# Performance work log

Measured on AMD Instinct MI355X. Metric: run time of the kernel, lower is better.

The kernel has to match this reference:

```python
import jax, jax.numpy as jnp
import numpy as np

N = 8192        # nodes
V = 50000       # vocab = len(dict_node_names)
EMB = 256       # embedding_dim
XI = EMB // 2   # x_increased_dim = 128
DIN = EMB + XI  # 384, SelfAtt_ dim
H = 4           # n_heads
D = 128         # WGAT output_dim per head (fusion dim)
E = 131072      # edges
CHUNK = 32768   # chunk_size (E % CHUNK == 0)


def _ln(x, g, b, eps=1e-5):
    m = jnp.mean(x, axis=-1, keepdims=True)
    v = jnp.mean((x - m) ** 2, axis=-1, keepdims=True)
    return (x - m) * jax.lax.rsqrt(v + eps) * g + b


def _wgat(emb, src, dst, edge_attr, wi, bi, wj, bj, wt, bt, attn):
    # x_i = features at destination (aggregation target), x_j = source/neighbor
    x_i = emb[dst]                                   # [E, din]
    x_j = emb[src]                                   # [E, din]
    h = (x_i @ wi + bi).reshape(E, H, D) + (x_j @ wj + bj).reshape(E, H, D)
    a = jnp.einsum('ehd,hd->eh', h, attn)            # [E, H]
    a = a * edge_attr[:, None]                       # edge weights pre-softmax
    # faithful chunked softmax: normalize over edges WITHIN each chunk (dim=0 per chunk)
    a = jax.nn.softmax(a.reshape(E // CHUNK, CHUNK, H), axis=1).reshape(E, H)
    xt = (x_j @ wt + bt).reshape(E, H, D)            # [E, H, D]
    msg = jnp.einsum('ehd,eh->ed', xt, a)            # sum over heads -> [E, D]
    return jax.ops.segment_sum(msg, dst, num_segments=N)  # aggr='add'


def _emb_forward(ids, edge_index, x, edge_attr, embed,
                 qkv_w, qkv_b, proj_w, proj_b, fuse_w, fuse_b, ln1_g, ln1_b,
                 wi0, bi0, wj0, bj0, wt0, bt0, attn0, skip0_w, skip0_b,
                 wi1, bi1, wj1, bj1, wt1, bt1, attn1, skip1_w, skip1_b,
                 ln2_g, ln2_b):
    E_i = embed[ids]                                 # [N, EMB] gather
    z = jnp.concatenate([jnp.tile(x, (1, XI)), E_i], axis=-1)   # [N, DIN]
    # SelfAtt_ : full N x N attention over nodes, scale = DIN**-0.5
    qkv = z @ qkv_w + qkv_b
    q, k, v = jnp.split(qkv, 3, axis=-1)
    att = jax.nn.softmax((q @ k.T) * (DIN ** -0.5), axis=-1) @ v
    z = att @ proj_w + proj_b                        # [N, DIN]
    emb = jax.nn.silu(_ln(z @ fuse_w + fuse_b, ln1_g, ln1_b)) + E_i  # [N, EMB]
    src, dst = edge_index[0], edge_index[1]
    emb = _wgat(emb, src, dst, edge_attr, wi0, bi0, wj0, bj0, wt0, bt0, attn0)  # [N, D]
    s0 = emb @ skip0_w + skip0_b
    emb = _wgat(emb, src, dst, edge_attr, wi1, bi1, wj1, bj1, wt1, bt1, attn1)  # [N, D]
    s1 = emb @ skip1_w + skip1_b
    emb = _ln(emb + (s0 + s1) * 0.5, ln2_g, ln2_b)
    return emb


def setup_inputs() -> dict:
    key = jax.random.key(0)
    ks = jax.random.split(key, 32)

    def w(k, shape, scale=0.05):
        return jax.random.normal(k, shape, jnp.float32) * scale

    inp = {}
    inp['ids'] = jax.random.randint(ks[0], (N,), 0, V)
    inp['x'] = jax.random.normal(ks[1], (N, 1), jnp.float32)
    inp['edge_attr'] = jax.random.uniform(ks[2], (E,), jnp.float32)
    inp['edge_index'] = jax.random.randint(ks[3], (2, E), 0, N)
    inp['embed'] = w(ks[4], (V, EMB), 1.0)
    inp['qkv_w'] = w(ks[5], (DIN, 3 * DIN)); inp['qkv_b'] = jnp.zeros((3 * DIN,), jnp.float32)
    inp['proj_w'] = w(ks[6], (DIN, DIN));    inp['proj_b'] = jnp.zeros((DIN,), jnp.float32)
    inp['fuse_w'] = w(ks[7], (DIN, EMB));    inp['fuse_b'] = jnp.zeros((EMB,), jnp.float32)
    inp['ln1_g'] = jnp.ones((EMB,), jnp.float32); inp['ln1_b'] = jnp.zeros((EMB,), jnp.float32)
    # WGAT layer 0: in=EMB, out=D per head, H heads
    inp['wi0'] = w(ks[8], (EMB, H * D));  inp['bi0'] = jnp.zeros((H * D,), jnp.float32)
    inp['wj0'] = w(ks[9], (EMB, H * D));  inp['bj0'] = jnp.zeros((H * D,), jnp.float32)
    inp['wt0'] = w(ks[10], (EMB, H * D)); inp['bt0'] = jnp.zeros((H * D,), jnp.float32)
    inp['attn0'] = w(ks[11], (H, D), 0.1)
    inp['skip0_w'] = w(ks[12], (D, D));   inp['skip0_b'] = jnp.zeros((D,), jnp.float32)
    # WGAT layer 1: in=D
    inp['wi1'] = w(ks[13], (D, H * D));   inp['bi1'] = jnp.zeros((H * D,), jnp.float32)
    inp['wj1'] = w(ks[14], (D, H * D));   inp['bj1'] = jnp.zeros((H * D,), jnp.float32)
    inp['wt1'] = w(ks[15], (D, H * D));   inp['bt1'] = jnp.zeros((H * D,), jnp.float32)
    inp['attn1'] = w(ks[16], (H, D), 0.1)
    inp['skip1_w'] = w(ks[17], (D, D));   inp['skip1_b'] = jnp.zeros((D,), jnp.float32)
    inp['ln2_g'] = jnp.ones((D,), jnp.float32); inp['ln2_b'] = jnp.zeros((D,), jnp.float32)
    return inp


def reference(ids, x, edge_attr, edge_index, embed,
              qkv_w, qkv_b, proj_w, proj_b, fuse_w, fuse_b, ln1_g, ln1_b,
              wi0, bi0, wj0, bj0, wt0, bt0, attn0, skip0_w, skip0_b,
              wi1, bi1, wj1, bj1, wt1, bt1, attn1, skip1_w, skip1_b,
              ln2_g, ln2_b):
    emb = _emb_forward(ids, edge_index, x, edge_attr, embed,
                       qkv_w, qkv_b, proj_w, proj_b, fuse_w, fuse_b, ln1_g, ln1_b,
                       wi0, bi0, wj0, bj0, wt0, bt0, attn0, skip0_w, skip0_b,
                       wi1, bi1, wj1, bj1, wt1, bt1, attn1, skip1_w, skip1_b,
                       ln2_g, ln2_b)
    return (emb, embed, ids)
```

## Files before the change

kernel.cpp:

```cpp
#include <hip/hip_runtime.h>

typedef __attribute__((ext_vector_type(8))) short bfrag;
typedef __attribute__((ext_vector_type(4))) float f4;

#define MFMA(a,b,c) __builtin_amdgcn_mfma_f32_16x16x32_bf16(a,b,c,0,0,0)

__device__ __forceinline__ unsigned short f2b(float x){
  union { float f; unsigned int u; } v; v.f = x;
  unsigned int r = v.u + 0x7fffu + ((v.u >> 16) & 1u);
  return (unsigned short)(r >> 16);
}
__device__ __forceinline__ float b2f(unsigned short h){
  union { unsigned int u; float f; } v; v.u = ((unsigned int)h) << 16;
  return v.f;
}

__global__ __launch_bounds__(256) void k_prep(
    const float* __restrict__ qkv_w, const float* __restrict__ proj_w,
    const float* __restrict__ proj_b, const float* __restrict__ fuse_w,
    const float* __restrict__ fuse_b,
    const float* __restrict__ wt0,
    const float* __restrict__ wt1, const float* __restrict__ sk0w,
    const float* __restrict__ wi0, const float* __restrict__ bi0,
    const float* __restrict__ wj0, const float* __restrict__ bj0,
    const float* __restrict__ wi1, const float* __restrict__ bi1,
    const float* __restrict__ wj1, const float* __restrict__ bj1,
    const float* __restrict__ attn0, const float* __restrict__ attn1,
    const float* __restrict__ bt0, const float* __restrict__ bt1,
    const float* __restrict__ sk0b,
    const float* __restrict__ embed, const int* __restrict__ ids,
    unsigned short* __restrict__ BtQKV, unsigned short* __restrict__ BtW2,
    unsigned short* __restrict__ BtT0, unsigned short* __restrict__ BtT1,
    float* __restrict__ biasW2,
    float* __restrict__ biasT0, float* __restrict__ biasT1,
    float* __restrict__ wsum, float* __restrict__ Ei)
{
  int b = blockIdx.x, t = threadIdx.x;
  if (b < 1152) {
    int idx = b*256 + t; int k = idx/1152, n = idx - k*1152;
    BtQKV[(size_t)n*256 + k] = f2b(qkv_w[128*1152 + idx]);
  } else if (b < 1536) {
    int k = b - 1152;
    float s = 0.f;
    for (int j = 0; j < 384; ++j) s += proj_w[(size_t)k*384 + j] * fuse_w[(size_t)j*256 + t];
    BtW2[(size_t)t*384 + k] = f2b(s);
  } else if (b == 1536) {
    float s = fuse_b[t];
    for (int j = 0; j < 384; ++j) s += proj_b[j] * fuse_w[(size_t)j*256 + t];
    biasW2[t] = s;
  } else if (b < 2049) {
    int idx = (b-1537)*256 + t; int k = idx/512, n = idx - k*512;
    BtT0[(size_t)n*256 + k] = f2b(wt0[idx]);
  } else if (b < 2305) {
    int idx = (b-2049)*256 + t; int k = idx/512, n = idx - k*512;
    BtT1[(size_t)n*128 + k] = f2b(wt1[idx]);
  } else if (b < 2369) {
    int idx = (b-2305)*256 + t; int k = idx/128, n = idx - k*128;
    BtT1[(size_t)(512+n)*128 + k] = f2b(sk0w[idx]);
  } else if (b < 2373) {
    int idx = (b-2369)*256 + t;
    int h = idx >> 8, k = idx & 255;
    float s = 0.f;
    for (int d = 0; d < 128; ++d) s += wi0[(size_t)k*512 + h*128 + d] * attn0[h*128 + d];
    BtT0[(size_t)(512 + h)*256 + k] = f2b(s);
    if (idx < 4) {
      float sb = 0.f;
      for (int d = 0; d < 128; ++d) sb += bi0[idx*128 + d] * attn0[idx*128 + d];
      biasT0[512 + idx] = sb;
    }
  } else if (b < 2377) {
    int idx = (b-2373)*256 + t;
    int h = idx >> 8, k = idx & 255;
    float s = 0.f;
    for (int d = 0; d < 128; ++d) s += wj0[(size_t)k*512 + h*128 + d] * attn0[h*128 + d];
    BtT0[(size_t)(516 + h)*256 + k] = f2b(s);
    if (idx < 4) {
      float sb = 0.f;
      for (int d = 0; d < 128; ++d) sb += bj0[idx*128 + d] * attn0[idx*128 + d];
      biasT0[516 + idx] = sb;
    }
  } else if (b < 2379) {
    int idx = (b-2377)*256 + t;
    int h = idx >> 7, k = idx & 127;
    float s = 0.f;
    for (int d = 0; d < 128; ++d) s += wi1[(size_t)k*512 + h*128 + d] * attn1[h*128 + d];
    BtT1[(size_t)(640 + h)*128 + k] = f2b(s);
    if (idx < 4) {
      float sb = 0.f;
      for (int d = 0; d < 128; ++d) sb += bi1[idx*128 + d] * attn1[idx*128 + d];
      biasT1[640 + idx] = sb;
    }
  } else if (b < 2381) {
    int idx = (b-2379)*256 + t;
    int h = idx >> 7, k = idx & 127;
    float s = 0.f;
    for (int d = 0; d < 128; ++d) s += wj1[(size_t)k*512 + h*128 + d] * attn1[h*128 + d];
    BtT1[(size_t)(644 + h)*128 + k] = f2b(s);
    if (idx < 4) {
      float sb = 0.f;
      for (int d = 0; d < 128; ++d) sb += bj1[idx*128 + d] * attn1[idx*128 + d];
      biasT1[644 + idx] = sb;
    }
  } else if (b < 2383) {
    int idx = (b-2381)*256 + t; biasT0[idx] = bt0[idx];
  } else if (b < 2385) {
    int idx = (b-2383)*256 + t; biasT1[idx] = bt1[idx];
  } else if (b == 2385) {
    if (t < 128) biasT1[512 + t] = sk0b[t];
  } else if (b < 2391) {
    int n = (b-2386)*256 + t;
    if (n < 1152) {
      float s = 0.f;
      for (int k = 0; k < 128; ++k) s += qkv_w[(size_t)k*1152 + n];
      wsum[n] = s;
    }
  } else {
    int idx = (b-2391)*256 + t;
    int n = idx >> 6, c4 = idx & 63;
    reinterpret_cast<float4*>(Ei)[idx] =
        reinterpret_cast<const float4*>(embed + (size_t)ids[n]*256)[c4];
  }
}

__global__ void k_outcopy(const float* __restrict__ embed, const int* __restrict__ ids,
                          float* __restrict__ out){
  int i = blockIdx.x*256 + threadIdx.x;
  if (i < 3200000)
    reinterpret_cast<float4*>(out)[262144 + i] = reinterpret_cast<const float4*>(embed)[i];
  if (i < 8192) out[13848576 + i] = (float)ids[i];
}

__global__ void k_deg(const int* __restrict__ ei, int* __restrict__ deg){
  int e = blockIdx.x*256 + threadIdx.x; if (e >= 131072) return;
  atomicAdd(&deg[ei[131072 + e]], 1);
}

__global__ __launch_bounds__(1024) void k_scan(const int* __restrict__ deg,
                                               int* __restrict__ off, int* __restrict__ cursor){
  int t = threadIdx.x;
  int v[8]; int s = 0;
  #pragma unroll
  for (int i=0;i<8;++i){ v[i] = s; s += deg[t*8 + i]; }
  int lane = t & 63, w = t >> 6;
  int si = s;
  for (int o=1;o<64;o<<=1){ int u = __shfl_up(si, o); if (lane >= o) si += u; }
  __shared__ int wsum[16];
  if (lane == 63) wsum[w] = si;
  __syncthreads();
  if (t < 16) {
    int x = wsum[t];
    for (int o=1;o<16;o<<=1){ int u = __shfl_up(x, o); if (t >= o) x += u; }
    wsum[t] = x;
  }
  __syncthreads();
  int wbase = (w == 0) ? 0 : wsum[w-1];
  int base = wbase + (si - s);
  #pragma unroll
  for (int i=0;i<8;++i){ int o2 = base + v[i]; off[t*8+i] = o2; cursor[t*8+i] = o2; }
  if (t == 1023) off[8192] = wbase + si;
}

__global__ void k_fill(const int* __restrict__ ei, int* __restrict__ cursor,
                       int* __restrict__ elist){
  int e = blockIdx.x*256 + threadIdx.x; if (e >= 131072) return;
  int d = ei[131072 + e];
  int slot = atomicAdd(&cursor[d], 1);
  elist[slot] = e;
}

__global__ __launch_bounds__(256) void k_gemm(
    const float* __restrict__ A, int lda,
    const unsigned short* __restrict__ Bt, int K,
    const float* __restrict__ bias,
    float* __restrict__ C, int ldc, int mode,
    const float* __restrict__ xv, const float* __restrict__ wsum,
    unsigned short* __restrict__ qO, unsigned short* __restrict__ kO,
    unsigned short* __restrict__ vO,
    const unsigned short* __restrict__ opA, const float* __restrict__ cw)
{
  __shared__ unsigned short As[128*40];
  __shared__ unsigned short Bs[128*40];
  const int t = threadIdx.x;
  const int wid = t >> 6, l = t & 63;
  const int lr = l & 15, lg = l >> 4;
  const int arow0 = blockIdx.y*128, bn0 = blockIdx.x*128;
  const int wr = (wid >> 1)*64, wc = (wid & 1)*64;
  f4 zero = {0.f,0.f,0.f,0.f};
  f4 acc[4][4];
  #pragma unroll
  for (int i=0;i<4;++i)
    #pragma unroll
    for (int j=0;j<4;++j) acc[i][j] = zero;

  for (int k0 = 0; k0 < K; k0 += 32) {
    #pragma unroll
    for (int p=0;p<4;++p) {
      int row = p*32 + (t>>3);
      int c4  = (t&7)*4;
      ushort4 h4;
      if (mode == 2) {
        const float* w4 = &cw[(arow0+row)*4];
        float a0=0.f,a1=0.f,a2=0.f,a3=0.f;
        #pragma unroll
        for (int s=0;s<4;++s) {
          ushort4 u = *reinterpret_cast<const ushort4*>(
              opA + (size_t)s*3145728 + (size_t)(arow0+row)*384 + k0 + c4);
          float wv = w4[s];
          a0 += b2f(u.x)*wv; a1 += b2f(u.y)*wv; a2 += b2f(u.z)*wv; a3 += b2f(u.w)*wv;
        }
        h4.x = f2b(a0); h4.y = f2b(a1); h4.z = f2b(a2); h4.w = f2b(a3);
      } else {
        float4 v = *reinterpret_cast<const float4*>(A + (size_t)(arow0+row)*lda + k0 + c4);
        h4.x = f2b(v.x); h4.y = f2b(v.y); h4.z = f2b(v.z); h4.w = f2b(v.w);
      }
      *reinterpret_cast<ushort4*>(&As[row*40 + c4]) = h4;
    }
    #pragma unroll
    for (int p=0;p<2;++p) {
      int n  = p*64 + (t>>2);
      int c8 = (t&3)*8;
      int4 v = *reinterpret_cast<const int4*>(Bt + (size_t)(bn0+n)*K + k0 + c8);
      *reinterpret_cast<int4*>(&Bs[n*40 + c8]) = v;
    }
    __syncthreads();
    bfrag af[4], bfm[4];
    #pragma unroll
    for (int mi=0;mi<4;++mi) af[mi] = *reinterpret_cast<const bfrag*>(&As[(wr+mi*16+lr)*40 + lg*8]);
    #pragma unroll
    for (int ni=0;ni<4;++ni) bfm[ni] = *reinterpret_cast<const bfrag*>(&Bs[(wc+ni*16+lr)*40 + lg*8]);
    #pragma unroll
    for (int mi=0;mi<4;++mi)
      #pragma unroll
      for (int ni=0;ni<4;++ni)
        acc[mi][ni] = MFMA(af[mi], bfm[ni], acc[mi][ni]);
    __syncthreads();
  }
  #pragma unroll
  for (int mi=0;mi<4;++mi) {
    #pragma unroll
    for (int ni=0;ni<4;++ni) {
      int col = bn0 + wc + ni*16 + lr;
      float bv = bias[col];
      float wsv = (mode==1) ? wsum[col] : 0.f;
      #pragma unroll
      for (int i=0;i<4;++i) {
        int row = arow0 + wr + mi*16 + lg*4 + i;
        float val = acc[mi][ni][i] + bv;
        if (mode == 1) {
          val += xv[row]*wsv;
          if (col < 384) val *= 0.05103103631f;
          unsigned short hv = f2b(val);
          if (col < 384)      qO[(size_t)row*384 + col] = hv;
          else if (col < 768) kO[(size_t)row*384 + col - 384] = hv;
          else {
            int d = col - 768, j = row;
            size_t vidx = (size_t)(j >> 5)*12288 + (size_t)(d >> 4)*512
                        + (size_t)(d & 15)*32 + (size_t)((j & 31) >> 3)*8 + (j & 7);
            vO[vidx] = hv;
          }
        } else {
          C[(size_t)row*ldc + col] = val;
        }
      }
    }
  }
}

__global__ __launch_bounds__(256,2) void k_flash(
    const unsigned short* __restrict__ qg,
    const unsigned short* __restrict__ kg,
    const unsigned short* __restrict__ vg,
    unsigned short* __restrict__ Opart, float* __restrict__ mpart, float* __restrict__ lpart)
{
  __shared__ unsigned short Ks[32*384];
  __shared__ unsigned short Ps[64*40];
  __shared__ float f_s[64];

  const int t = threadIdx.x;
  const int w = t >> 6, l = t & 63;
  const int lr = l & 15, lg = l >> 4;
  const int qbi = blockIdx.x >> 2, split = blockIdx.x & 3;
  const int qbase = qbi * 64;

  #define STAGE_K(JJ) do { \
    _Pragma("unroll") \
    for (int p_=0;p_<6;++p_) { \
      int idx_ = p_*256 + t; \
      int row_ = idx_ / 48, uu_ = idx_ - row_*48; \
      int ug_ = uu_ ^ (row_ & 7); \
      const unsigned short* gp_ = kg + (size_t)((JJ) + row_)*384 + ug_*8; \
      __builtin_amdgcn_global_load_lds((const __attribute__((address_space(1))) void*)gp_, \
          (__attribute__((address_space(3))) void*)&Ks[idx_*8], 16, 0, 0); \
    } } while(0)

  bfrag qf[12];
  #pragma unroll
  for (int kk=0;kk<12;++kk)
    qf[kk] = *reinterpret_cast<const bfrag*>(qg + (size_t)(qbase + w*16 + lr)*384 + kk*32 + lg*8);

  f4 zero = {0.f,0.f,0.f,0.f};
  f4 o[4][6];
  #pragma unroll
  for (int a=0;a<4;++a)
    #pragma unroll
    for (int b=0;b<6;++b) o[a][b] = zero;

  float m = -3e38f, lsum = 0.f;
  const int j0beg = split*2048, jend = j0beg + 2048;

  STAGE_K(j0beg);
  __syncthreads();

  for (int j0 = j0beg; j0 < jend; j0 += 32) {
    f4 s0 = zero, s1 = zero;
    __builtin_amdgcn_s_setprio(1);
    #pragma unroll
    for (int kk=0;kk<12;++kk) {
      int su = ((kk*4 + lg) ^ (lr & 7)) * 8;
      bfrag k0 = *reinterpret_cast<const bfrag*>(&Ks[lr*384 + su]);
      bfrag k1 = *reinterpret_cast<const bfrag*>(&Ks[(16+lr)*384 + su]);
      s0 = MFMA(k0, qf[kk], s0);
      s1 = MFMA(k1, qf[kk], s1);
    }
    __builtin_amdgcn_s_setprio(0);

    float mt = fmaxf(fmaxf(fmaxf(s0[0],s0[1]),fmaxf(s0[2],s0[3])),
                     fmaxf(fmaxf(s1[0],s1[1]),fmaxf(s1[2],s1[3])));
    mt = fmaxf(mt, __shfl_xor(mt,16));
    mt = fmaxf(mt, __shfl_xor(mt,32));
    bool grew = mt > m + 8.f;
    bool doresc = __any(grew);
    float mn = doresc ? fmaxf(m, mt) : m;
    float p0[4], p1[4];
    float sum = 0.f;
    #pragma unroll
    for (int i=0;i<4;++i) {
      p0[i] = __expf(s0[i]-mn); p1[i] = __expf(s1[i]-mn);
      sum += p0[i] + p1[i];
    }
    sum += __shfl_xor(sum,16);
    sum += __shfl_xor(sum,32);
    float f = 1.f;
    if (doresc) {
      f = __expf(m - mn);
      lsum = lsum * f + sum;
      m = mn;
    } else {
      lsum += sum;
    }

    unsigned int pk0 = (unsigned int)f2b(p0[0]) | ((unsigned int)f2b(p0[1]) << 16);
    unsigned int pk1 = (unsigned int)f2b(p0[2]) | ((unsigned int)f2b(p0[3]) << 16);
    unsigned int pk2 = (unsigned int)f2b(p1[0]) | ((unsigned int)f2b(p1[1]) << 16);
    unsigned int pk3 = (unsigned int)f2b(p1[2]) | ((unsigned int)f2b(p1[3]) << 16);
    int prow = (w*16 + lr)*40;
    *reinterpret_cast<unsigned int*>(&Ps[prow + lg*4])          = pk0;
    *reinterpret_cast<unsigned int*>(&Ps[prow + lg*4 + 2])      = pk1;
    *reinterpret_cast<unsigned int*>(&Ps[prow + 16 + lg*4])     = pk2;
    *reinterpret_cast<unsigned int*>(&Ps[prow + 16 + lg*4 + 2]) = pk3;
    if (lg == 0) f_s[w*16 + lr] = f;

    __syncthreads();

    if (j0 + 32 < jend) STAGE_K(j0 + 32);

    const int jt = j0 >> 5;
    bfrag vf[6];
    #pragma unroll
    for (int dt=0;dt<6;++dt)
      vf[dt] = *reinterpret_cast<const bfrag*>(
          vg + (size_t)jt*12288 + (size_t)(w*6 + dt)*512 + lr*32 + lg*8);

    bfrag pf[4];
    #pragma unroll
    for (int qt=0;qt<4;++qt)
      pf[qt] = *reinterpret_cast<const bfrag*>(&Ps[(qt*16+lr)*40 + lg*8]);
    #pragma unroll
    for (int qt=0;qt<4;++qt) {
      #pragma unroll
      for (int i=0;i<4;++i) {
        float frv = f_s[qt*16 + lg*4 + i];
        #pragma unroll
        for (int dt=0;dt<6;++dt) o[qt][dt][i] *= frv;
      }
    }
    __builtin_amdgcn_s_setprio(1);
    #pragma unroll
    for (int qt=0;qt<4;++qt)
      #pragma unroll
      for (int dt=0;dt<6;++dt)
        o[qt][dt] = MFMA(pf[qt], vf[dt], o[qt][dt]);
    __builtin_amdgcn_s_setprio(0);

    __syncthreads();
  }
  #undef STAGE_K

  unsigned short* Op = Opart + (size_t)split*8192*384;
  #pragma unroll
  for (int qt=0;qt<4;++qt)
    #pragma unroll
    for (int dt=0;dt<6;++dt)
      #pragma unroll
      for (int i=0;i<4;++i)
        Op[(size_t)(qbase + qt*16 + lg*4 + i)*384 + w*96 + dt*16 + lr] = f2b(o[qt][dt][i]);
  if (lg == 0) {
    mpart[split*8192 + qbase + w*16 + lr] = m;
    lpart[split*8192 + qbase + w*16 + lr] = lsum;
  }
}

__global__ void k_cw(const float* __restrict__ mp, const float* __restrict__ lp,
                     float* __restrict__ cw)
{
  int r = blockIdx.x*256 + threadIdx.x;
  float m0 = mp[r], m1 = mp[8192+r], m2 = mp[16384+r], m3 = mp[24576+r];
  float M = fmaxf(fmaxf(m0,m1), fmaxf(m2,m3));
  float w0 = __expf(m0-M), w1 = __expf(m1-M), w2 = __expf(m2-M), w3 = __expf(m3-M);
  float L = lp[r]*w0 + lp[8192+r]*w1 + lp[16384+r]*w2 + lp[24576+r]*w3;
  float inv = 1.f / L;
  float4 o4 = make_float4(w0*inv, w1*inv, w2*inv, w3*inv);
  *reinterpret_cast<float4*>(&cw[r*4]) = o4;
}

__global__ __launch_bounds__(256) void k_ln1(const float* __restrict__ pre, const float* __restrict__ Ei,
                      const float* __restrict__ g, const float* __restrict__ b,
                      float* __restrict__ out)
{
  int row = blockIdx.x, c = threadIdx.x;
  float v = pre[(size_t)row*256 + c];
  float s1 = v, s2 = v*v;
  #pragma unroll
  for (int o1=32;o1;o1>>=1){ s1 += __shfl_down(s1,o1); s2 += __shfl_down(s2,o1); }
  __shared__ float a1[4], a2[4];
  if ((c&63)==0){ a1[c>>6] = s1; a2[c>>6] = s2; }
  __syncthreads();
  float S1 = a1[0]+a1[1]+a1[2]+a1[3], S2 = a2[0]+a2[1]+a2[2]+a2[3];
  float mean = S1*(1.f/256.f), var = S2*(1.f/256.f) - mean*mean;
  float y = (v-mean)*rsqrtf(var+1e-5f)*g[c] + b[c];
  float sig = 1.f/(1.f+__expf(-y));
  out[(size_t)row*256 + c] = y*sig + Ei[(size_t)row*256 + c];
}

__global__ void k_escore(const int* __restrict__ ei, const float* __restrict__ ea,
                         const float* __restrict__ TC, int ldc, int aoff,
                         float* __restrict__ sc)
{
  int e = blockIdx.x*256 + threadIdx.x; if (e >= 131072) return;
  int s = ei[e], d = ei[131072 + e];
  float wv = ea[e];
  #pragma unroll
  for (int h=0; h<4; ++h) {
    float ai = TC[(size_t)d*ldc + aoff + h];
    float aj = TC[(size_t)s*ldc + aoff + 4 + h];
    sc[e*4 + h] = (ai + aj) * wv;
  }
}

__global__ __launch_bounds__(1024) void k_cstats(const float* __restrict__ sc,
                        float* __restrict__ mx, float* __restrict__ sm)
{
  int ch = blockIdx.x;
  int c = ch >> 2, h = ch & 3;
  int t = threadIdx.x;
  const float* base = sc + (size_t)c*131072 + h;
  float lm = -3e38f, ls = 0.f;
  for (int i=t; i<32768; i+=1024) {
    float v = base[(size_t)i*4];
    if (v > lm) { ls = ls*__expf(lm - v) + 1.f; lm = v; }
    else        ls += __expf(v - lm);
  }
  #pragma unroll
  for (int o1=32;o1;o1>>=1) {
    float om = __shfl_down(lm,o1), os = __shfl_down(ls,o1);
    float M2 = fmaxf(lm, om);
    ls = ls*__expf(lm-M2) + os*__expf(om-M2);
    lm = M2;
  }
  __shared__ float rm[16], rs[16];
  if ((t&63)==0){ rm[t>>6] = lm; rs[t>>6] = ls; }
  __syncthreads();
  if (t == 0) {
    float M = rm[0], S = rs[0];
    for (int i=1;i<16;++i) {
      float M2 = fmaxf(M, rm[i]);
      S = S*__expf(M-M2) + rs[i]*__expf(rm[i]-M2);
      M = M2;
    }
    mx[ch] = M; sm[ch] = S;
  }
}

__global__ void k_pnorm(float* __restrict__ sc, const float* __restrict__ mx,
                        const float* __restrict__ sm)
{
  int i = blockIdx.x*256 + threadIdx.x;
  int e = i >> 2, h = i & 3;
  int ch = (e >> 15)*4 + h;
  sc[i] = __expf(sc[i] - mx[ch]) / sm[ch];
}

__global__ __launch_bounds__(128) void k_aggr(const int* __restrict__ off,
                      const int* __restrict__ elist, const int* __restrict__ ei,
                      const float* __restrict__ sc,
                      const float* __restrict__ TC, int ldc, float* __restrict__ g)
{
  int n = blockIdx.x, d = threadIdx.x;
  int qb = off[n], qe = off[n+1];
  float acc = 0.f;
  for (int q = qb; q < qe; ++q) {
    int e = elist[q];
    int s = ei[e];
    float4 p = *reinterpret_cast<const float4*>(&sc[e*4]);
    const float* Tr = TC + (size_t)s*ldc;
    acc += p.x*Tr[d] + p.y*Tr[128+d] + p.z*Tr[256+d] + p.w*Tr[384+d];
  }
  g[(size_t)n*128 + d] = acc;
}

__global__ __launch_bounds__(128) void k_final(const float* __restrict__ g1, const float* __restrict__ TC1,
                       const float* __restrict__ sw, const float* __restrict__ sb,
                       const float* __restrict__ lg2, const float* __restrict__ lb2,
                       float* __restrict__ out)
{
  int row = blockIdx.x, c = threadIdx.x;
  __shared__ float gr[128];
  float gv = g1[(size_t)row*128 + c];
  gr[c] = gv; __syncthreads();
  float s1 = sb[c];
  #pragma unroll 8
  for (int k=0;k<128;++k) s1 += gr[k]*sw[k*128 + c];
  float s0 = TC1[(size_t)row*768 + 512 + c];
  float v = gv + 0.5f*(s0 + s1);
  float m1 = v, m2 = v*v;
  #pragma unroll
  for (int o1=32;o1;o1>>=1){ m1 += __shfl_down(m1,o1); m2 += __shfl_down(m2,o1); }
  __shared__ float a1[2], a2[2];
  if ((c&63)==0){ a1[c>>6]=m1; a2[c>>6]=m2; }
  __syncthreads();
  float S1 = a1[0]+a1[1], S2 = a2[0]+a2[1];
  float mean = S1*(1.f/128.f), var = S2*(1.f/128.f) - mean*mean;
  out[(size_t)row*128 + c] = (v-mean)*rsqrtf(var+1e-5f)*lg2[c] + lb2[c];
}

extern "C" void kernel_launch(void* const* d_in, const int* in_sizes, int n_in,
                              void* d_out, int out_size, void* d_ws, size_t ws_size,
                              hipStream_t stream)
{
  const int*   ids    = (const int*)  d_in[0];
  const float* x      = (const float*)d_in[1];
  const float* ea     = (const float*)d_in[2];
  const int*   eidx   = (const int*)  d_in[3];
  const float* embed  = (const float*)d_in[4];
  const float* qkv_w  = (const float*)d_in[5];
  const float* qkv_b  = (const float*)d_in[6];
  const float* proj_w = (const float*)d_in[7];
  const float* proj_b = (const float*)d_in[8];
  const float* fuse_w = (const float*)d_in[9];
  const float* fuse_b = (const float*)d_in[10];
  const float* ln1_g  = (const float*)d_in[11];
  const float* ln1_b  = (const float*)d_in[12];
  const float* wi0 = (const float*)d_in[13]; const float* bi0 = (const float*)d_in[14];
  const float* wj0 = (const float*)d_in[15]; const float* bj0 = (const float*)d_in[16];
  const float* wt0 = (const float*)d_in[17]; const float* bt0 = (const float*)d_in[18];
  const float* attn0 = (const float*)d_in[19];
  const float* sk0w = (const float*)d_in[20]; const float* sk0b = (const float*)d_in[21];
  const float* wi1 = (const float*)d_in[22]; const float* bi1 = (const float*)d_in[23];
  const float* wj1 = (const float*)d_in[24]; const float* bj1 = (const float*)d_in[25];
  const float* wt1 = (const float*)d_in[26]; const float* bt1 = (const float*)d_in[27];
  const float* attn1 = (const float*)d_in[28];
  const float* sk1w = (const float*)d_in[29]; const float* sk1b = (const float*)d_in[30];
  const float* ln2_g = (const float*)d_in[31]; const float* ln2_b = (const float*)d_in[32];

  char* ws = (char*)d_ws;
  const size_t MBy = (size_t)1 << 20;

  unsigned short* BtQKV  = (unsigned short*)(ws + 0);
  unsigned short* BtW2   = (unsigned short*)(ws + 589824);
  float* biasW2 = (float*)(ws + 884736);
  unsigned short* BtT0   = (unsigned short*)(ws + 1081344);
  unsigned short* BtT1   = (unsigned short*)(ws + 1409024);
  float* biasT0 = (float*)(ws + 1605632);
  float* biasT1 = (float*)(ws + 1608192);
  float* wsum   = (float*)(ws + 1611264);
  float* mxb    = (float*)(ws + 1615872);
  float* smb    = (float*)(ws + 1615936);
  int* deg    = (int*)(ws + 1703936);
  int* cursor = (int*)(ws + 1736704);
  int* off    = (int*)(ws + 1769472);
  float* cw   = (float*)(ws + 1806336);

  float* Ei   = (float*)(ws + 2*MBy);
  unsigned short* qb = (unsigned short*)(ws + 10*MBy);
  unsigned short* kb = (unsigned short*)(ws + 17*MBy);
  unsigned short* vb = (unsigned short*)(ws + 24*MBy);
  float* pre  = (float*)(ws + 45*MBy);
  float* emb0 = (float*)(ws + 31*MBy);
  float* TC0  = (float*)(ws + 43*MBy);
  float* sc0  = (float*)(ws + 26*MBy);
  float* g0   = (float*)(ws + 2*MBy);
  float* TC1  = (float*)(ws + 6*MBy);
  float* sc1  = (float*)(ws + 43*MBy);
  float* g1   = (float*)(ws + 47448064);
  int* elist  = (int*)(ws + 64*MBy);

  float* out = (float*)d_out;
  unsigned short* Opart = (unsigned short*)d_out;
  float* mpart = out + 6815744;
  float* lpart = out + 6848512;

  hipMemsetAsync(ws, 0, 2*MBy, stream);

  k_prep<<<4439, 256, 0, stream>>>(qkv_w, proj_w, proj_b, fuse_w, fuse_b,
                                   wt0, wt1, sk0w,
                                   wi0, bi0, wj0, bj0, wi1, bi1, wj1, bj1,
                                   attn0, attn1, bt0, bt1, sk0b, embed, ids,
                                   BtQKV, BtW2, BtT0, BtT1,
                                   biasW2, biasT0, biasT1, wsum, Ei);
  k_deg<<<512, 256, 0, stream>>>(eidx, deg);
  k_scan<<<1, 1024, 0, stream>>>(deg, off, cursor);
  k_fill<<<512, 256, 0, stream>>>(eidx, cursor, elist);

  k_gemm<<<dim3(9,64), 256, 0, stream>>>(Ei, 256, BtQKV, 256, qkv_b, nullptr, 0, 1,
                                         x, wsum, qb, kb, vb, nullptr, nullptr);
  k_flash<<<512, 256, 0, stream>>>(qb, kb, vb, Opart, mpart, lpart);
  k_cw<<<32, 256, 0, stream>>>(mpart, lpart, cw);

  k_gemm<<<dim3(2,64), 256, 0, stream>>>(nullptr, 0, BtW2, 384, biasW2, pre, 256, 2,
                                         nullptr, nullptr, nullptr, nullptr, nullptr,
                                         Opart, cw);
  k_outcopy<<<12500, 256, 0, stream>>>(embed, ids, out);
  k_ln1<<<8192, 256, 0, stream>>>(pre, Ei, ln1_g, ln1_b, emb0);

  k_gemm<<<dim3(5,64), 256, 0, stream>>>(emb0, 256, BtT0, 256, biasT0, TC0, 640, 0,
                                         nullptr, nullptr, nullptr, nullptr, nullptr,
                                         nullptr, nullptr);
  k_escore<<<512, 256, 0, stream>>>(eidx, ea, TC0, 640, 512, sc0);
  k_cstats<<<16, 1024, 0, stream>>>(sc0, mxb, smb);
  k_pnorm<<<2048, 256, 0, stream>>>(sc0, mxb, smb);
  k_aggr<<<8192, 128, 0, stream>>>(off, elist, eidx, sc0, TC0, 640, g0);

  k_gemm<<<dim3(6,64), 256, 0, stream>>>(g0, 128, BtT1, 128, biasT1, TC1, 768, 0,
                                         nullptr, nullptr, nullptr, nullptr, nullptr,
                                         nullptr, nullptr);
  k_escore<<<512, 256, 0, stream>>>(eidx, ea, TC1, 768, 640, sc1);
  k_cstats<<<16, 1024, 0, stream>>>(sc1, mxb, smb);
  k_pnorm<<<2048, 256, 0, stream>>>(sc1, mxb, smb);
  k_aggr<<<8192, 128, 0, stream>>>(off, elist, eidx, sc1, TC1, 768, g1);

  k_final<<<8192, 128, 0, stream>>>(g1, TC1, sk1w, sk1b, ln2_g, ln2_b, out);
}
```

Before: 467.1 us.

## Split WGAT GEMM outputs into bf16 transform, compact score, and skip buffers

Adds a GEMM epilogue mode that writes the per-head transformed features as bf16 in a dense 512-wide layout. It writes the eight attention-score columns into a compact 8-float-per-node array and the skip projection into a separate auxiliary buffer. The edge-score kernel now reads the scores with float4 loads, and aggregation gathers bf16 rows. Together these cut the bytes moved by the gather-heavy edge kernels. The cost is bf16 rounding of the messages and a reshuffled workspace layout with more aliasing to get right.

```diff
diff --git a/kernel.cpp b/kernel.cpp
--- a/kernel.cpp
+++ b/kernel.cpp
@@ -56,7 +56,7 @@
     BtT1[(size_t)n*128 + k] = f2b(wt1[idx]);
   } else if (b < 2369) {
     int idx = (b-2305)*256 + t; int k = idx/128, n = idx - k*128;
-    BtT1[(size_t)(512+n)*128 + k] = f2b(sk0w[idx]);
+    BtT1[(size_t)(520+n)*128 + k] = f2b(sk0w[idx]);
   } else if (b < 2373) {
     int idx = (b-2369)*256 + t;
     int h = idx >> 8, k = idx & 255;
@@ -84,29 +84,29 @@
     int h = idx >> 7, k = idx & 127;
     float s = 0.f;
     for (int d = 0; d < 128; ++d) s += wi1[(size_t)k*512 + h*128 + d] * attn1[h*128 + d];
-    BtT1[(size_t)(640 + h)*128 + k] = f2b(s);
+    BtT1[(size_t)(512 + h)*128 + k] = f2b(s);
     if (idx < 4) {
       float sb = 0.f;
       for (int d = 0; d < 128; ++d) sb += bi1[idx*128 + d] * attn1[idx*128 + d];
-      biasT1[640 + idx] = sb;
+      biasT1[512 + idx] = sb;
     }
   } else if (b < 2381) {
     int idx = (b-2379)*256 + t;
     int h = idx >> 7, k = idx & 127;
     float s = 0.f;
     for (int d = 0; d < 128; ++d) s += wj1[(size_t)k*512 + h*128 + d] * attn1[h*128 + d];
-    BtT1[(size_t)(644 + h)*128 + k] = f2b(s);
+    BtT1[(size_t)(516 + h)*128 + k] = f2b(s);
     if (idx < 4) {
       float sb = 0.f;
       for (int d = 0; d < 128; ++d) sb += bj1[idx*128 + d] * attn1[idx*128 + d];
-      biasT1[644 + idx] = sb;
+      biasT1[516 + idx] = sb;
     }
   } else if (b < 2383) {
     int idx = (b-2381)*256 + t; biasT0[idx] = bt0[idx];
   } else if (b < 2385) {
     int idx = (b-2383)*256 + t; biasT1[idx] = bt1[idx];
   } else if (b == 2385) {
-    if (t < 128) biasT1[512 + t] = sk0b[t];
+    if (t < 128) biasT1[520 + t] = sk0b[t];
   } else if (b < 2391) {
     int n = (b-2386)*256 + t;
     if (n < 1152) {
@@ -176,7 +176,8 @@
     const float* __restrict__ xv, const float* __restrict__ wsum,
     unsigned short* __restrict__ qO, unsigned short* __restrict__ kO,
     unsigned short* __restrict__ vO,
-    const unsigned short* __restrict__ opA, const float* __restrict__ cw)
+    const unsigned short* __restrict__ opA, const float* __restrict__ cw,
+    float* __restrict__ aux, int ncols)
 {
   __shared__ unsigned short As[128*40];
   __shared__ unsigned short Bs[128*40];
@@ -258,6 +259,10 @@
                         + (size_t)(d & 15)*32 + (size_t)((j & 31) >> 3)*8 + (j & 7);
             vO[vidx] = hv;
           }
+        } else if (mode == 3) {
+          if (col < 512)      qO[(size_t)row*512 + col] = f2b(val);
+          else if (col < 520) C[(size_t)row*8 + col - 512] = val;
+          else if (col < ncols) aux[(size_t)row*128 + col - 520] = val;
         } else {
           C[(size_t)row*ldc + col] = val;
         }
@@ -443,18 +448,15 @@
 }
 
 __global__ void k_escore(const int* __restrict__ ei, const float* __restrict__ ea,
-                         const float* __restrict__ TC, int ldc, int aoff,
-                         float* __restrict__ sc)
+                         const float* __restrict__ SC, float* __restrict__ sc)
 {
   int e = blockIdx.x*256 + threadIdx.x; if (e >= 131072) return;
   int s = ei[e], d = ei[131072 + e];
   float wv = ea[e];
-  #pragma unroll
-  for (int h=0; h<4; ++h) {
-    float ai = TC[(size_t)d*ldc + aoff + h];
-    float aj = TC[(size_t)s*ldc + aoff + 4 + h];
-    sc[e*4 + h] = (ai + aj) * wv;
-  }
+  float4 ai = *reinterpret_cast<const float4*>(&SC[(size_t)d*8]);
+  float4 aj = *reinterpret_cast<const float4*>(&SC[(size_t)s*8 + 4]);
+  float4 o4 = make_float4((ai.x+aj.x)*wv, (ai.y+aj.y)*wv, (ai.z+aj.z)*wv, (ai.w+aj.w)*wv);
+  *reinterpret_cast<float4*>(&sc[e*4]) = o4;
 }
 
 __global__ __launch_bounds__(1024) void k_cstats(const float* __restrict__ sc,
@@ -503,7 +505,7 @@
 __global__ __launch_bounds__(128) void k_aggr(const int* __restrict__ off,
                       const int* __restrict__ elist, const int* __restrict__ ei,
                       const float* __restrict__ sc,
-                      const float* __restrict__ TC, int ldc, float* __restrict__ g)
+                      const unsigned short* __restrict__ Tb, float* __restrict__ g)
 {
   int n = blockIdx.x, d = threadIdx.x;
   int qb = off[n], qe = off[n+1];
@@ -512,13 +514,13 @@
     int e = elist[q];
     int s = ei[e];
     float4 p = *reinterpret_cast<const float4*>(&sc[e*4]);
-    const float* Tr = TC + (size_t)s*ldc;
-    acc += p.x*Tr[d] + p.y*Tr[128+d] + p.z*Tr[256+d] + p.w*Tr[384+d];
+    const unsigned short* Tr = Tb + (size_t)s*512;
+    acc += p.x*b2f(Tr[d]) + p.y*b2f(Tr[128+d]) + p.z*b2f(Tr[256+d]) + p.w*b2f(Tr[384+d]);
   }
   g[(size_t)n*128 + d] = acc;
 }
 
-__global__ __launch_bounds__(128) void k_final(const float* __restrict__ g1, const float* __restrict__ TC1,
+__global__ __launch_bounds__(128) void k_final(const float* __restrict__ g1, const float* __restrict__ aux,
                        const float* __restrict__ sw, const float* __restrict__ sb,
                        const float* __restrict__ lg2, const float* __restrict__ lb2,
                        float* __restrict__ out)
@@ -530,7 +532,7 @@
   float s1 = sb[c];
   #pragma unroll 8
   for (int k=0;k<128;++k) s1 += gr[k]*sw[k*128 + c];
-  float s0 = TC1[(size_t)row*768 + 512 + c];
+  float s0 = aux[(size_t)row*128 + c];
   float v = gv + 0.5f*(s0 + s1);
   float m1 = v, m2 = v*v;
   #pragma unroll
@@ -594,15 +596,18 @@
   unsigned short* qb = (unsigned short*)(ws + 10*MBy);
   unsigned short* kb = (unsigned short*)(ws + 17*MBy);
   unsigned short* vb = (unsigned short*)(ws + 24*MBy);
-  float* pre  = (float*)(ws + 45*MBy);
-  float* emb0 = (float*)(ws + 31*MBy);
-  float* TC0  = (float*)(ws + 43*MBy);
-  float* sc0  = (float*)(ws + 26*MBy);
+  float* pre  = (float*)(ws + 31*MBy);
+  float* emb0 = (float*)(ws + 39*MBy);
+  unsigned short* TCb0 = (unsigned short*)(ws + 47*MBy);
+  float* SCb0 = (float*)(ws + 55*MBy);
+  float* SCb1 = (float*)(ws + 55*MBy + 262144);
+  float* AUX  = (float*)(ws + 56*MBy);
+  float* sc0  = (float*)(ws + 60*MBy);
+  unsigned short* TCb1 = (unsigned short*)(ws + 10*MBy);
+  float* sc1  = (float*)(ws + 24*MBy);
   float* g0   = (float*)(ws + 2*MBy);
-  float* TC1  = (float*)(ws + 6*MBy);
-  float* sc1  = (float*)(ws + 43*MBy);
-  float* g1   = (float*)(ws + 47448064);
-  int* elist  = (int*)(ws + 64*MBy);
+  float* g1   = (float*)(ws + 6*MBy);
+  int* elist  = (int*)(ws + 62*MBy);
 
   float* out = (float*)d_out;
   unsigned short* Opart = (unsigned short*)d_out;
@@ -622,31 +627,32 @@
   k_fill<<<512, 256, 0, stream>>>(eidx, cursor, elist);
 
   k_gemm<<<dim3(9,64), 256, 0, stream>>>(Ei, 256, BtQKV, 256, qkv_b, nullptr, 0, 1,
-                                         x, wsum, qb, kb, vb, nullptr, nullptr);
+                                         x, wsum, qb, kb, vb, nullptr, nullptr,
+                                         nullptr, 0);
   k_flash<<<512, 256, 0, stream>>>(qb, kb, vb, Opart, mpart, lpart);
   k_cw<<<32, 256, 0, stream>>>(mpart, lpart, cw);
 
   k_gemm<<<dim3(2,64), 256, 0, stream>>>(nullptr, 0, BtW2, 384, biasW2, pre, 256, 2,
                                          nullptr, nullptr, nullptr, nullptr, nullptr,
-                                         Opart, cw);
+                                         Opart, cw, nullptr, 0);
   k_outcopy<<<12500, 256, 0, stream>>>(embed, ids, out);
   k_ln1<<<8192, 256, 0, stream>>>(pre, Ei, ln1_g, ln1_b, emb0);
 
-  k_gemm<<<dim3(5,64), 256, 0, stream>>>(emb0, 256, BtT0, 256, biasT0, TC0, 640, 0,
-                                         nullptr, nullptr, nullptr, nullptr, nullptr,
-                                         nullptr, nullptr);
-  k_escore<<<512, 256, 0, stream>>>(eidx, ea, TC0, 640, 512, sc0);
+  k_gemm<<<dim3(5,64), 256, 0, stream>>>(emb0, 256, BtT0, 256, biasT0, SCb0, 0, 3,
+                                         nullptr, nullptr, TCb0, nullptr, nullptr,
+                                         nullptr, nullptr, AUX, 520);
+  k_escore<<<512, 256, 0, stream>>>(eidx, ea, SCb0, sc0);
   k_cstats<<<16, 1024, 0, stream>>>(sc0, mxb, smb);
   k_pnorm<<<2048, 256, 0, stream>>>(sc0, mxb, smb);
-  k_aggr<<<8192, 128, 0, stream>>>(off, elist, eidx, sc0, TC0, 640, g0);
-
-  k_gemm<<<dim3(6,64), 256, 0, stream>>>(g0, 128, BtT1, 128, biasT1, TC1, 768, 0,
-                                         nullptr, nullptr, nullptr, nullptr, nullptr,
-                                         nullptr, nullptr);
-  k_escore<<<512, 256, 0, stream>>>(eidx, ea, TC1, 768, 640, sc1);
+  k_aggr<<<8192, 128, 0, stream>>>(off, elist, eidx, sc0, TCb0, g0);
+
+  k_gemm<<<dim3(6,64), 256, 0, stream>>>(g0, 128, BtT1, 128, biasT1, SCb1, 0, 3,
+                                         nullptr, nullptr, TCb1, nullptr, nullptr,
+                                         nullptr, nullptr, AUX, 648);
+  k_escore<<<512, 256, 0, stream>>>(eidx, ea, SCb1, sc1);
   k_cstats<<<16, 1024, 0, stream>>>(sc1, mxb, smb);
   k_pnorm<<<2048, 256, 0, stream>>>(sc1, mxb, smb);
-  k_aggr<<<8192, 128, 0, stream>>>(off, elist, eidx, sc1, TC1, 768, g1);
-
-  k_final<<<8192, 128, 0, stream>>>(g1, TC1, sk1w, sk1b, ln2_g, ln2_b, out);
-}
+  k_aggr<<<8192, 128, 0, stream>>>(off, elist, eidx, sc1, TCb1, g1);
+
+  k_final<<<8192, 128, 0, stream>>>(g1, AUX, sk1w, sk1b, ln2_g, ln2_b, out);
+}
```

Measured after the change: 458.6 us. About the same (-1.8%).
